# Kernel optimization log

Measured on AMD Instinct MI355X. Metric: run time of the kernel, lower is better.

## Reference

```python
import jax, jax.numpy as jnp
import numpy as np

jax.config.update("jax_enable_x64", True)  # original module computes in float64

N_ITER = 25      # fixed interior-point iterations (replaces maxIter-driven loop)
SIGMA = 0.1      # centering parameter
FTB = 0.99       # fraction-to-boundary factor
NX = 64          # (n^2)^3 with n=2
M_EQ = 40        # rows of A (SUDOKU_MATRIX_SHAPE)
BATCH = 1024


def setup_inputs() -> dict:
    key = jax.random.key(0)
    k1, k2 = jax.random.split(key)
    puzzles = jax.random.uniform(k1, (BATCH, 4, 4, 4), dtype=jnp.float32)
    # learned parameters (as in QPLayer.__init__)
    A = jax.random.uniform(k2, (M_EQ, NX), dtype=jnp.float64)
    log_z0 = jnp.zeros((NX,), dtype=jnp.float64)
    # fixed buffers
    Q = jnp.zeros((NX, NX), dtype=jnp.float64)
    G = -jnp.eye(NX, dtype=jnp.float64)
    u = jnp.zeros((NX,), dtype=jnp.float64)
    return {"puzzles": puzzles, "A": A, "log_z0": log_z0, "Q": Q, "G": G, "u": u}


def _solve_qp(Q, p, A, b, G, u):
    """Primal-dual interior-point solve of
        min 1/2 x^T Q x + p^T x  s.t.  A x = b,  G x <= u
    (lower bound l=-1e20 in the original is inactive). p is batched [B,nx]."""
    nx, m_eq, m_in = Q.shape[0], A.shape[0], G.shape[0]

    def solve_one(p_i):
        x0 = jnp.zeros((nx,), Q.dtype)
        y0 = jnp.zeros((m_eq,), Q.dtype)
        s0 = jnp.ones((m_in,), Q.dtype)
        z0 = jnp.ones((m_in,), Q.dtype)

        def step(carry, _):
            x, y, s, z = carry
            rd = Q @ x + p_i + A.T @ y + G.T @ z        # dual residual
            rp = A @ x - b                              # primal eq residual
            rs = G @ x + s - u                          # primal ineq residual
            mu = jnp.dot(s, z) / m_in
            w = z / s
            # reduced KKT: [Q + G^T W G, A^T; A, 0] [dx; dy] = [rhs_x; -rp]
            rhs_x = -(rd + G.T @ ((SIGMA * mu - z * s + z * rs) / s))
            M = Q + G.T @ (w[:, None] * G)
            KKT = jnp.block([[M, A.T], [A, jnp.zeros((m_eq, m_eq), Q.dtype)]])
            rhs = jnp.concatenate([rhs_x, -rp])
            sol = jnp.linalg.solve(KKT, rhs)
            dx, dy = sol[:nx], sol[nx:]
            ds = -rs - G @ dx
            dz = (SIGMA * mu - z * s + z * rs) / s + w * (G @ dx)
            # fraction-to-boundary step to keep s,z > 0
            def max_step(v, dv):
                ratio = jnp.where(dv < 0, -v / dv, jnp.inf)
                return jnp.minimum(1.0, FTB * jnp.min(ratio))
            alpha = jnp.minimum(max_step(s, ds), max_step(z, dz))
            return (x + alpha * dx, y + alpha * dy,
                    s + alpha * ds, z + alpha * dz), None

        (x, _, _, _), _ = jax.lax.scan(step, (x0, y0, s0, z0), None, length=N_ITER)
        return x

    return jax.vmap(solve_one)(p)


def reference(puzzles, A, log_z0, Q, G, u):
    n_batch = puzzles.shape[0]
    p = -puzzles.reshape(n_batch, -1).astype(jnp.float64)   # p = -puzzles.view(B,-1)
    b = A @ jnp.exp(log_z0)                                  # b = A @ exp(log_z0)
    x = _solve_qp(Q, p, A, b, G, u)                          # [B, nx] float64
    return x.astype(jnp.float32).reshape(puzzles.shape)
```

## Files before the change

### kernel.cpp

```cpp
#include <hip/hip_runtime.h>
#include <math.h>


#define NXV   64
#define MEQ   40
#define NITER 25
#define SIGMA_C 0.1
#define FTB_C   0.99
#define SA 65
#define SS 41
#define PIV_DROP_REL 1e-12

typedef double f64x16 __attribute__((ext_vector_type(16)));
typedef double f64x8  __attribute__((ext_vector_type(8)));

union DU { double d; int i[2]; unsigned u[2]; };

__device__ __forceinline__ double readlane_f64(double v, int lane) {
    DU a; a.d = v; DU r;
    r.i[0] = __builtin_amdgcn_readlane(a.i[0], lane);
    r.i[1] = __builtin_amdgcn_readlane(a.i[1], lane);
    return r.d;
}

template<int CTRL>
__device__ __forceinline__ double dpp_add_step(double v) {
    DU a; a.d = v; DU b;
    b.i[0] = __builtin_amdgcn_update_dpp(0, a.i[0], CTRL, 0xf, 0xf, true);
    b.i[1] = __builtin_amdgcn_update_dpp(0, a.i[1], CTRL, 0xf, 0xf, true);
    return v + b.d;
}
__device__ __forceinline__ double wave_sum_f64(double v) {
    v = dpp_add_step<0x111>(v); v = dpp_add_step<0x112>(v);
    v = dpp_add_step<0x114>(v); v = dpp_add_step<0x118>(v);
    v = dpp_add_step<0x142>(v); v = dpp_add_step<0x143>(v);
    return readlane_f64(v, 63);
}
template<int CTRL>
__device__ __forceinline__ double dpp_min_step(double v) {
    DU a; a.d = v; DU b;
    b.i[0] = __builtin_amdgcn_update_dpp(0x00000000, a.i[0], CTRL, 0xf, 0xf, false);
    b.i[1] = __builtin_amdgcn_update_dpp(0x7ff00000, a.i[1], CTRL, 0xf, 0xf, false);
    return fmin(v, b.d);
}
__device__ __forceinline__ double wave_min_f64(double v) {
    v = dpp_min_step<0x111>(v); v = dpp_min_step<0x112>(v);
    v = dpp_min_step<0x114>(v); v = dpp_min_step<0x118>(v);
    v = dpp_min_step<0x142>(v); v = dpp_min_step<0x143>(v);
    return readlane_f64(v, 63);
}
template<int CTRL>
__device__ __forceinline__ double dpp_max_step(double v) {
    DU a; a.d = v; DU b;
    b.i[0] = __builtin_amdgcn_update_dpp(0x00000000, a.i[0], CTRL, 0xf, 0xf, false);
    b.i[1] = __builtin_amdgcn_update_dpp((int)0xfff00000u, a.i[1], CTRL, 0xf, 0xf, false);
    return fmax(v, b.d);
}
__device__ __forceinline__ double wave_max_f64(double v) {
    v = dpp_max_step<0x111>(v); v = dpp_max_step<0x112>(v);
    v = dpp_max_step<0x114>(v); v = dpp_max_step<0x118>(v);
    v = dpp_max_step<0x142>(v); v = dpp_max_step<0x143>(v);
    return readlane_f64(v, 63);
}
template<int CTRL>
__device__ __forceinline__ unsigned dpp_maxu_step(unsigned v) {
    unsigned m = (unsigned)__builtin_amdgcn_update_dpp(0, (int)v, CTRL, 0xf, 0xf, true);
    return v > m ? v : m;
}
__device__ __forceinline__ unsigned wave_max_u32(unsigned v) {
    v = dpp_maxu_step<0x111>(v); v = dpp_maxu_step<0x112>(v);
    v = dpp_maxu_step<0x114>(v); v = dpp_maxu_step<0x118>(v);
    const unsigned a = (unsigned)__builtin_amdgcn_readlane((int)v, 15);
    const unsigned b = (unsigned)__builtin_amdgcn_readlane((int)v, 31);
    const unsigned c = (unsigned)__builtin_amdgcn_readlane((int)v, 47);
    const unsigned d = (unsigned)__builtin_amdgcn_readlane((int)v, 63);
    const unsigned ab = a > b ? a : b;
    const unsigned cd = c > d ? c : d;
    return ab > cd ? ab : cd;
}

#define P3_STEP(T, CUR, NXT)                                                  \
  do {                                                                        \
    const int t_ = (T);                                                       \
    double cL[24];                             \
    _Pragma("unroll")                               \
    for (int j = 0; j < 24; ++j) cL[j] = CUR[16 + j];                         \
    const double Lm_ = (diag_r > -1.0e307 && tid != kt) ? colreg * invP : 0.0;\
    if (tid < MEQ) Sl[t_ * SS + tid] = Lm_;  \
    diag_r -= Lm_ * colreg;                         \
    if (tid == kt) diag_r = -1.0e308;                         \
    const double fyk_ = readlane_f64(fy_r, kt);                               \
    fy_r -= Lm_ * fyk_;                             \
    DU dd_; dd_.d = diag_r;                                                   \
    const unsigned h_  = dd_.u[1];                                            \
    const unsigned mk_ = (h_ & 0x80000000u) ? ~h_ : (h_ | 0x80000000u);       \
    const unsigned key_ = wave_max_u32((mk_ & 0xFFFFFFC0u) | (unsigned)tid);  \
    const int ktn_ = (int)(key_ & 63u);                                       \
    const double pivn_ = readlane_f64(diag_r, ktn_);                          \
    double ipn_ = 1.0 / pivn_;                                                \
    ipn_ = (pivn_ > thr) ? ipn_ : 0.0;                 \
    if (tid == t_ + 1 && tid < MEQ) { kk_own = ktn_; ip_own = ipn_; }         \
       \
    const double e0 = Sg0[ktn_ & 15];                 \
    const double e1 = Sg1[(ktn_ - 16) & 15];                                  \
    const double e2 = Sg2[(ktn_ - 32) & 7];                                   \
    const double epre = (ktn_ < 16) ? e0 : ((ktn_ < 32) ? e1 : e2);           \
    const double cs = readlane_f64(colreg, ktn_);      \
    const double coln = epre - Lm_ * cs;          \
    NXT[tid] = coln;                            \
                    \
    _Pragma("unroll")                                                         \
    for (int j = 0; j < 16; ++j) Sg0[j] -= Lm_ * readlane_f64(colreg, j);     \
                      \
    _Pragma("unroll")                                                         \
    for (int j = 0; j < 16; ++j) Sg1[j] -= Lm_ * cL[j];                       \
    _Pragma("unroll")                                                         \
    for (int j = 0; j < 8; ++j)  Sg2[j] -= Lm_ * cL[16 + j];                  \
    colreg = coln;                                                            \
    kt = ktn_; invP = ipn_;                                                   \
  } while (0)

__global__ __launch_bounds__(64, 1)
void qp_ipm_kernel(const float* __restrict__ puzzles,
                   const float* __restrict__ Af,
                   const float* __restrict__ lzf,
                   const float* __restrict__ uf,
                   float* __restrict__ out)
{
    __shared__ double Ald[MEQ * SA];
    __shared__ double Sl[MEQ * SS];
    __shared__ __align__(16) double SrowA[NXV];
    __shared__ __align__(16) double SrowB[NXV];

    const int tid = threadIdx.x;
    const int b   = blockIdx.x;
    const int row = (tid < MEQ) ? tid : 0;

    for (int e = tid; e < MEQ * NXV; e += 64)
        Ald[(e >> 6) * SA + (e & 63)] = (double)Af[e];
    const double ez = exp((double)lzf[tid]);
    __syncthreads();
    double b0 = 0.0, b1 = 0.0, b2 = 0.0, b3 = 0.0;
    #pragma unroll
    for (int i = 0; i < NXV; i += 4) {
        b0 += Ald[row * SA + i + 0] * readlane_f64(ez, i + 0);
        b1 += Ald[row * SA + i + 1] * readlane_f64(ez, i + 1);
        b2 += Ald[row * SA + i + 2] * readlane_f64(ez, i + 2);
        b3 += Ald[row * SA + i + 3] * readlane_f64(ez, i + 3);
    }
    const double b_r = (b0 + b1) + (b2 + b3);

    const double u_i = (double)uf[tid];
    const double p_i = -(double)puzzles[b * NXV + tid];
    double x_r = 0.0, s_r = 1.0, z_r = 1.0, y_r = 0.0;

    for (int it = 0; it < NITER; ++it) {
        double at0 = 0.0, at1 = 0.0, at2 = 0.0, at3 = 0.0;
        #pragma unroll
        for (int j = 0; j < MEQ; j += 4) {
            at0 += Ald[(j + 0) * SA + tid] * readlane_f64(y_r, j + 0);
            at1 += Ald[(j + 1) * SA + tid] * readlane_f64(y_r, j + 1);
            at2 += Ald[(j + 2) * SA + tid] * readlane_f64(y_r, j + 2);
            at3 += Ald[(j + 3) * SA + tid] * readlane_f64(y_r, j + 3);
        }
        const double aty = (at0 + at1) + (at2 + at3);
        const double rd = p_i + aty - z_r;
        const double rs = s_r - x_r - u_i;
        const double mu = wave_sum_f64(s_r * z_r) * (1.0 / 64.0);
        const double rc = (SIGMA_C * mu - z_r * s_r + z_r * rs) / s_r;
        const double rx = rc - rd;
        const double d_r = s_r / z_r;
        const double v_r = d_r * rx + x_r;

        double f0 = 0.0, f1 = 0.0, f2 = 0.0, f3 = 0.0;
        #pragma unroll
        for (int i = 0; i < NXV; i += 4) {
            f0 += Ald[row * SA + i + 0] * readlane_f64(v_r, i + 0);
            f1 += Ald[row * SA + i + 1] * readlane_f64(v_r, i + 1);
            f2 += Ald[row * SA + i + 2] * readlane_f64(v_r, i + 2);
            f3 += Ald[row * SA + i + 3] * readlane_f64(v_r, i + 3);
        }
        double fy_r = (f0 + f1) + (f2 + f3) - b_r;

        if (tid < 55) {
            int uu = tid, mb = 0;
            while (uu > mb) { uu -= (mb + 1); ++mb; }
            const int nb = uu;
            double a00=0,a01=0,a02=0,a03=0, a10=0,a11=0,a12=0,a13=0,
                   a20=0,a21=0,a22=0,a23=0, a30=0,a31=0,a32=0,a33=0;
            const double* Am = &Ald[(4 * mb) * SA];
            const double* An = &Ald[(4 * nb) * SA];
            #pragma unroll 2
            for (int k = 0; k < NXV; ++k) {
                const double dk = readlane_f64(d_r, k);
                const double r0 = Am[0*SA+k], r1 = Am[1*SA+k], r2 = Am[2*SA+k], r3 = Am[3*SA+k];
                const double c0 = An[0*SA+k]*dk, c1 = An[1*SA+k]*dk, c2 = An[2*SA+k]*dk, c3 = An[3*SA+k]*dk;
                a00 += r0*c0; a01 += r0*c1; a02 += r0*c2; a03 += r0*c3;
                a10 += r1*c0; a11 += r1*c1; a12 += r1*c2; a13 += r1*c3;
                a20 += r2*c0; a21 += r2*c1; a22 += r2*c2; a23 += r2*c3;
                a30 += r3*c0; a31 += r3*c1; a32 += r3*c2; a33 += r3*c3;
            }
            double* Sp = &Sl[(4 * mb) * SS + 4 * nb];
            Sp[0*SS+0]=a00; Sp[0*SS+1]=a01; Sp[0*SS+2]=a02; Sp[0*SS+3]=a03;
            Sp[1*SS+0]=a10; Sp[1*SS+1]=a11; Sp[1*SS+2]=a12; Sp[1*SS+3]=a13;
            Sp[2*SS+0]=a20; Sp[2*SS+1]=a21; Sp[2*SS+2]=a22; Sp[2*SS+3]=a23;
            Sp[3*SS+0]=a30; Sp[3*SS+1]=a31; Sp[3*SS+2]=a32; Sp[3*SS+3]=a33;
            if (mb != nb) {
                double* Sq = &Sl[(4 * nb) * SS + 4 * mb];
                Sq[0*SS+0]=a00; Sq[1*SS+0]=a01; Sq[2*SS+0]=a02; Sq[3*SS+0]=a03;
                Sq[0*SS+1]=a10; Sq[1*SS+1]=a11; Sq[2*SS+1]=a12; Sq[3*SS+1]=a13;
                Sq[0*SS+2]=a20; Sq[1*SS+2]=a21; Sq[2*SS+2]=a22; Sq[3*SS+2]=a23;
                Sq[0*SS+3]=a30; Sq[1*SS+3]=a31; Sq[2*SS+3]=a32; Sq[3*SS+3]=a33;
            }
        }
        __syncthreads();

        f64x16 Sg0, Sg1; f64x8 Sg2;
        double diag_r;
        if (tid < MEQ) {
            #pragma unroll
            for (int j = 0; j < 16; ++j) Sg0[j] = Sl[tid * SS + j];
            #pragma unroll
            for (int j = 0; j < 16; ++j) Sg1[j] = Sl[tid * SS + 16 + j];
            #pragma unroll
            for (int j = 0; j < 8; ++j)  Sg2[j] = Sl[tid * SS + 32 + j];
            diag_r = Sl[tid * SS + tid];
        } else {
            #pragma unroll
            for (int j = 0; j < 16; ++j) { Sg0[j] = 0.0; Sg1[j] = 0.0; }
            #pragma unroll
            for (int j = 0; j < 8; ++j)  Sg2[j] = 0.0;
            diag_r = -1.0e308;
        }
        const double dg  = wave_max_f64(diag_r);
        const double thr = dg * PIV_DROP_REL;
        __syncthreads();

        double ip_own = 0.0;
        int    kk_own = tid;
        int    kt;  double invP, colreg;
        {
            DU dd; dd.d = diag_r;
            const unsigned h  = dd.u[1];
            const unsigned mk = (h & 0x80000000u) ? ~h : (h | 0x80000000u);
            const unsigned key = wave_max_u32((mk & 0xFFFFFFC0u) | (unsigned)tid);
            kt = (int)(key & 63u);
            const double piv = readlane_f64(diag_r, kt);
            double ip = 1.0 / piv;
            ip = (piv > thr) ? ip : 0.0;
            invP = ip;
            if (tid == 0) { kk_own = kt; ip_own = ip; }
            const double e0 = Sg0[kt & 15];
            const double e1 = Sg1[(kt - 16) & 15];
            const double e2 = Sg2[(kt - 32) & 7];
            colreg = (kt < 16) ? e0 : ((kt < 32) ? e1 : e2);
            SrowA[tid] = colreg;
        }
        for (int t = 0; t < MEQ; t += 2) {
            P3_STEP(t,     SrowA, SrowB);
            P3_STEP(t + 1, SrowB, SrowA);
        }

        double fyp;
        {
            DU a; a.d = fy_r; DU r;
            const int ad = kk_own << 2;
            r.i[0] = __builtin_amdgcn_ds_bpermute(ad, a.i[0]);
            r.i[1] = __builtin_amdgcn_ds_bpermute(ad, a.i[1]);
            fyp = r.d;
        }
        const double rhs = fyp * ip_own;
        #pragma unroll
        for (int t = 0; t < 16; ++t) {
            const int kts = __builtin_amdgcn_readlane(kk_own, t);
            Sg0[t] = Sl[row * SS + kts];
        }
        #pragma unroll
        for (int t = 0; t < 16; ++t) {
            const int kts = __builtin_amdgcn_readlane(kk_own, 16 + t);
            Sg1[t] = Sl[row * SS + kts];
        }
        #pragma unroll
        for (int t = 0; t < 8; ++t) {
            const int kts = __builtin_amdgcn_readlane(kk_own, 32 + t);
            Sg2[t] = Sl[row * SS + kts];
        }
        double resid = rhs;
        #pragma unroll
        for (int t = MEQ - 1; t >= 32; --t) {
            const double xt = readlane_f64(resid, t);
            resid -= Sg2[t - 32] * xt;
        }
        #pragma unroll
        for (int t = 31; t >= 16; --t) {
            const double xt = readlane_f64(resid, t);
            resid -= Sg1[t - 16] * xt;
        }
        #pragma unroll
        for (int t = 15; t >= 0; --t) {
            const double xt = readlane_f64(resid, t);
            resid -= Sg0[t] * xt;
        }
        double X_r;
        {
            DU a; a.d = resid; DU r;
            const int ad = kk_own << 2;
            r.i[0] = __builtin_amdgcn_ds_permute(ad, a.i[0]);
            r.i[1] = __builtin_amdgcn_ds_permute(ad, a.i[1]);
            X_r = r.d;
        }

        double ad0 = 0.0, ad1 = 0.0, ad2 = 0.0, ad3 = 0.0;
        #pragma unroll
        for (int j = 0; j < MEQ; j += 4) {
            ad0 += Ald[(j + 0) * SA + tid] * readlane_f64(X_r, j + 0);
            ad1 += Ald[(j + 1) * SA + tid] * readlane_f64(X_r, j + 1);
            ad2 += Ald[(j + 2) * SA + tid] * readlane_f64(X_r, j + 2);
            ad3 += Ald[(j + 3) * SA + tid] * readlane_f64(X_r, j + 3);
        }
        const double atdy = (ad0 + ad1) + (ad2 + ad3);
        const double dx = d_r * (rx - atdy);
        const double ds = dx - rs;
        const double dz = rc - (z_r / s_r) * dx;
        double r = 1.0e300;
        if (ds < 0.0) r = -s_r / ds;
        if (dz < 0.0) r = fmin(r, -z_r / dz);
        r = wave_min_f64(r);
        const double alpha = fmin(1.0, FTB_C * r);
        x_r += alpha * dx;
        s_r += alpha * ds;
        z_r += alpha * dz;
        y_r += alpha * X_r;
    }

    out[b * NXV + tid] = (float)x_r;
}

extern "C" void kernel_launch(void* const* d_in, const int* in_sizes, int n_in,
                              void* d_out, int out_size, void* d_ws, size_t ws_size,
                              hipStream_t stream) {
    const float* puzzles = (const float*)d_in[0];
    const float* A       = (const float*)d_in[1];
    const float* logz0   = (const float*)d_in[2];
    const float* u       = (const float*)d_in[5];
    float* out = (float*)d_out;

    const int n_batch = in_sizes[0] / NXV;
    qp_ipm_kernel<<<n_batch, 64, 0, stream>>>(puzzles, A, logz0, u, out);
}
```

Before: 704.9 us.

## Split Schur-complement accumulation across a second helper wavefront per block

The block grows from one wave to two. The second wave computes the k=32..63 half of the A·D·Aᵀ products from a shared-memory copy of d, while the first wave computes k=0..31 and then adds the partial sums. This roughly halves the serial FMA work in the dominant per-iteration product. In exchange it adds several block barriers per iteration, with a fixed barrier count that has to match the hidden factorization code, and doubles the waves per block.

Measured after the change: 1.280 ms. +81.6%, slower.

```diff
diff --git a/kernel.cpp b/kernel.cpp
--- a/kernel.cpp
+++ b/kernel.cpp
@@ -120,7 +120,7 @@
     kt = ktn_; invP = ipn_;                                                   \
   } while (0)
 
-__global__ __launch_bounds__(64, 1)
+__global__ __launch_bounds__(128, 1)
 void qp_ipm_kernel(const float* __restrict__ puzzles,
                    const float* __restrict__ Af,
                    const float* __restrict__ lzf,
@@ -131,15 +131,53 @@
     __shared__ double Sl[MEQ * SS];
     __shared__ __align__(16) double SrowA[NXV];
     __shared__ __align__(16) double SrowB[NXV];
-
-    const int tid = threadIdx.x;
-    const int b   = blockIdx.x;
-    const int row = (tid < MEQ) ? tid : 0;
-
-    for (int e = tid; e < MEQ * NXV; e += 64)
+    __shared__ double dl[NXV];
+
+    const int t128 = threadIdx.x;
+    const int wid  = t128 >> 6;
+    const int tid  = t128 & 63;
+    const int b    = blockIdx.x;
+    const int row  = (tid < MEQ) ? tid : 0;
+
+    for (int e = t128; e < MEQ * NXV; e += 128)
         Ald[(e >> 6) * SA + (e & 63)] = (double)Af[e];
+    __syncthreads();
+
+    if (wid == 1) {
+        int uu = tid, mb = 0;
+        while (uu > mb) { uu -= (mb + 1); ++mb; }
+        const int nb = uu;
+        const double* Am = &Ald[(4 * mb) * SA];
+        const double* An = &Ald[(4 * nb) * SA];
+        double* Sp = &Sl[(4 * mb) * SS + 4 * nb];
+        for (int it = 0; it < NITER; ++it) {
+            __syncthreads();
+            if (tid < 55) {
+                double a00=0,a01=0,a02=0,a03=0, a10=0,a11=0,a12=0,a13=0,
+                       a20=0,a21=0,a22=0,a23=0, a30=0,a31=0,a32=0,a33=0;
+                #pragma unroll 2
+                for (int k = 32; k < 64; ++k) {
+                    const double dk = dl[k];
+                    const double r0 = Am[0*SA+k], r1 = Am[1*SA+k], r2 = Am[2*SA+k], r3 = Am[3*SA+k];
+                    const double c0 = An[0*SA+k]*dk, c1 = An[1*SA+k]*dk, c2 = An[2*SA+k]*dk, c3 = An[3*SA+k]*dk;
+                    a00 += r0*c0; a01 += r0*c1; a02 += r0*c2; a03 += r0*c3;
+                    a10 += r1*c0; a11 += r1*c1; a12 += r1*c2; a13 += r1*c3;
+                    a20 += r2*c0; a21 += r2*c1; a22 += r2*c2; a23 += r2*c3;
+                    a30 += r3*c0; a31 += r3*c1; a32 += r3*c2; a33 += r3*c3;
+                }
+                Sp[0*SS+0]=a00; Sp[0*SS+1]=a01; Sp[0*SS+2]=a02; Sp[0*SS+3]=a03;
+                Sp[1*SS+0]=a10; Sp[1*SS+1]=a11; Sp[1*SS+2]=a12; Sp[1*SS+3]=a13;
+                Sp[2*SS+0]=a20; Sp[2*SS+1]=a21; Sp[2*SS+2]=a22; Sp[2*SS+3]=a23;
+                Sp[3*SS+0]=a30; Sp[3*SS+1]=a31; Sp[3*SS+2]=a32; Sp[3*SS+3]=a33;
+            }
+            __syncthreads();
+            __syncthreads();
+            __syncthreads();
+        }
+        return;
+    }
+
     const double ez = exp((double)lzf[tid]);
-    __syncthreads();
     double b0 = 0.0, b1 = 0.0, b2 = 0.0, b3 = 0.0;
     #pragma unroll
     for (int i = 0; i < NXV; i += 4) {
@@ -171,6 +209,7 @@
         const double rx = rc - rd;
         const double d_r = s_r / z_r;
         const double v_r = d_r * rx + x_r;
+        dl[tid] = d_r;
 
         double f0 = 0.0, f1 = 0.0, f2 = 0.0, f3 = 0.0;
         #pragma unroll
@@ -181,17 +220,18 @@
             f3 += Ald[row * SA + i + 3] * readlane_f64(v_r, i + 3);
         }
         double fy_r = (f0 + f1) + (f2 + f3) - b_r;
-
+        __syncthreads();
+
+        int uu = tid, mb = 0;
+        while (uu > mb) { uu -= (mb + 1); ++mb; }
+        const int nb = uu;
+        double a00=0,a01=0,a02=0,a03=0, a10=0,a11=0,a12=0,a13=0,
+               a20=0,a21=0,a22=0,a23=0, a30=0,a31=0,a32=0,a33=0;
         if (tid < 55) {
-            int uu = tid, mb = 0;
-            while (uu > mb) { uu -= (mb + 1); ++mb; }
-            const int nb = uu;
-            double a00=0,a01=0,a02=0,a03=0, a10=0,a11=0,a12=0,a13=0,
-                   a20=0,a21=0,a22=0,a23=0, a30=0,a31=0,a32=0,a33=0;
             const double* Am = &Ald[(4 * mb) * SA];
             const double* An = &Ald[(4 * nb) * SA];
             #pragma unroll 2
-            for (int k = 0; k < NXV; ++k) {
+            for (int k = 0; k < 32; ++k) {
                 const double dk = readlane_f64(d_r, k);
                 const double r0 = Am[0*SA+k], r1 = Am[1*SA+k], r2 = Am[2*SA+k], r3 = Am[3*SA+k];
                 const double c0 = An[0*SA+k]*dk, c1 = An[1*SA+k]*dk, c2 = An[2*SA+k]*dk, c3 = An[3*SA+k]*dk;
@@ -200,7 +240,15 @@
                 a20 += r2*c0; a21 += r2*c1; a22 += r2*c2; a23 += r2*c3;
                 a30 += r3*c0; a31 += r3*c1; a32 += r3*c2; a33 += r3*c3;
             }
+        }
+        __syncthreads();
+
+        if (tid < 55) {
             double* Sp = &Sl[(4 * mb) * SS + 4 * nb];
+            a00 += Sp[0*SS+0]; a01 += Sp[0*SS+1]; a02 += Sp[0*SS+2]; a03 += Sp[0*SS+3];
+            a10 += Sp[1*SS+0]; a11 += Sp[1*SS+1]; a12 += Sp[1*SS+2]; a13 += Sp[1*SS+3];
+            a20 += Sp[2*SS+0]; a21 += Sp[2*SS+1]; a22 += Sp[2*SS+2]; a23 += Sp[2*SS+3];
+            a30 += Sp[3*SS+0]; a31 += Sp[3*SS+1]; a32 += Sp[3*SS+2]; a33 += Sp[3*SS+3];
             Sp[0*SS+0]=a00; Sp[0*SS+1]=a01; Sp[0*SS+2]=a02; Sp[0*SS+3]=a03;
             Sp[1*SS+0]=a10; Sp[1*SS+1]=a11; Sp[1*SS+2]=a12; Sp[1*SS+3]=a13;
             Sp[2*SS+0]=a20; Sp[2*SS+1]=a21; Sp[2*SS+2]=a22; Sp[2*SS+3]=a23;
@@ -213,7 +261,6 @@
                 Sq[0*SS+3]=a30; Sq[1*SS+3]=a31; Sq[2*SS+3]=a32; Sq[3*SS+3]=a33;
             }
         }
-        __syncthreads();
 
         f64x16 Sg0, Sg1; f64x8 Sg2;
         double diag_r;
@@ -331,6 +378,7 @@
         s_r += alpha * ds;
         z_r += alpha * dz;
         y_r += alpha * X_r;
+        __syncthreads();
     }
 
     out[b * NXV + tid] = (float)x_r;
@@ -346,5 +394,5 @@
     float* out = (float*)d_out;
 
     const int n_batch = in_sizes[0] / NXV;
-    qp_ipm_kernel<<<n_batch, 64, 0, stream>>>(puzzles, A, logz0, u, out);
-}
+    qp_ipm_kernel<<<n_batch, 128, 0, stream>>>(puzzles, A, logz0, u, out);
+}
```
